# Performance work log

Measured on AMD Instinct MI355X. Metric: run time of the kernel, lower is better.

Reference implementation:

```python
import jax, jax.numpy as jnp
import numpy as np

BLOCK_SIZE = 32
BLOCK_COUNTS = 16
B, N, H, D = 4, 1024, 8, 64
LENGTHS = np.array([1024, 768, 512, 896], dtype=np.int64)


def setup_inputs() -> dict:
    key = jax.random.key(0)
    ks = jax.random.split(key, 8)
    offsets = np.concatenate([[0], np.cumsum(LENGTHS)]).astype(np.int32)
    mask = np.zeros((B, N), dtype=bool)
    for b in range(B):
        mask[b, : int(LENGTHS[b])] = True
    gather_idx = np.nonzero(mask.reshape(-1))[0].astype(np.int32)
    m = jnp.asarray(mask)[:, :, None, None].astype(jnp.float32)
    padded_q = jax.random.normal(ks[0], (B, N, H, D), jnp.float32) * m
    padded_k = jax.random.normal(ks[1], (B, N, H, D), jnp.float32) * m
    padded_v = jax.random.normal(ks[2], (B, N, H, D), jnp.float32) * m
    gidx = jnp.asarray(gather_idx)
    jagged_q = padded_q.reshape(B * N, H, D)[gidx]
    jagged_k = padded_k.reshape(B * N, H, D)[gidx]
    jagged_v = padded_v.reshape(B * N, H, D)[gidx]
    jagged_u = jax.random.normal(ks[3], (int(gidx.shape[0]), H, D), jnp.float32)
    gate_w = jax.random.normal(ks[4], (H, D, 3), jnp.float32) * 0.1
    return {"jagged_q": jagged_q, "jagged_k": jagged_k, "jagged_v": jagged_v,
            "jagged_u": jagged_u, "padded_q": padded_q, "padded_k": padded_k,
            "padded_v": padded_v, "x_offsets": jnp.asarray(offsets),
            "gate_w": gate_w, "padding_mask": jnp.asarray(mask),
            "gather_idx": gidx}


def _forward(jagged_q, jagged_k, jagged_v, padded_q, padded_k, padded_v,
             x_offsets, gate_w, gather_idx):
    scale = D ** -0.5
    nb = N // BLOCK_SIZE                                   # N is a multiple of BLOCK_SIZE (pad_len=0)
    S = min(BLOCK_COUNTS, nb)
    lengths = x_offsets[1:] - x_offsets[:-1]               # [B]
    cmp_len = (lengths + BLOCK_SIZE - 1) // BLOCK_SIZE     # [B] valid compressed blocks per seq
    pos = jnp.arange(N)
    blk = jnp.arange(nb)
    q_blk = pos // BLOCK_SIZE

    # scatter jagged tokens back to dense padded layout (zeros at padding) --
    # the Triton kernels read q/k/v from the jagged tensors.
    def to_dense(j):
        return jnp.zeros((B * N, H, D), j.dtype).at[gather_idx].set(j).reshape(B, N, H, D)
    qd, kd, vd = to_dense(jagged_q), to_dense(jagged_k), to_dense(jagged_v)

    # gates: per-token/per-head sigmoid linear gate from padded_q -> (g_cmp, g_slc, g_swa)
    gates = jax.nn.sigmoid(jnp.einsum('bnhd,hdg->bnhg', padded_q, gate_w))
    g_cmp, g_slc = gates[..., 0], gates[..., 1]            # g_swa unused by this module

    # compressed (block-mean) keys / values  [B, nb, H, D]
    k_cmp = padded_k.reshape(B, nb, BLOCK_SIZE, H, D).mean(axis=2)
    v_cmp = padded_v.reshape(B, nb, BLOCK_SIZE, H, D).mean(axis=2)

    # ---- compressed branch: SiLU attention over block-mean keys ----
    s_cmp = jnp.einsum('bqhd,bkhd->bqhk', qd, k_cmp) * scale          # [B,N,H,nb]
    mask_cmp = (q_blk[:, None] >= blk[None, :])[None, :, None, :] & \
               (blk[None, None, None, :] < cmp_len[:, None, None, None])
    p_cmp = jnp.where(mask_cmp, jax.nn.silu(s_cmp), 0.0)
    o_cmp = jnp.einsum('bqhk,bkhd->bqhd', p_cmp, v_cmp) * g_cmp[..., None]

    # ---- block selection: causal top-k over compressed scores ----
    s_sel = jnp.einsum('bqhd,bkhd->bhqk', padded_q, k_cmp) * scale    # [B,H,N,nb]
    causal_blk = (q_blk[:, None] >= blk[None, :])[None, None]
    _, top_idx = jax.lax.top_k(jnp.where(causal_blk, s_sel, -jnp.inf), S)  # [B,H,N,S]
    top_idx = jnp.where(top_idx > q_blk[None, None, :, None], -1, top_idx)
    top_idx = top_idx.transpose(0, 2, 1, 3)                           # [B,N,H,S]

    # ---- selected branch: SiLU attention restricted to selected blocks ----
    blk_sel = jnp.any(top_idx[..., None] == blk, axis=-2)             # [B,N,H,nb] (-1 matches nothing)
    key_sel = jnp.repeat(blk_sel, BLOCK_SIZE, axis=-1)                # [B,N,H,N]
    mask_slc = key_sel & (pos[:, None] >= pos[None, :])[None, :, None, :]
    s_slc = jnp.einsum('bqhd,bkhd->bqhk', qd, kd) * scale             # [B,N,H,N]
    p_slc = jnp.where(mask_slc, jax.nn.silu(s_slc), 0.0)
    o_slc = jnp.einsum('bqhk,bkhd->bqhd', p_slc, vd) * g_slc[..., None]

    # jagged output: gather valid tokens
    return (o_cmp + o_slc).reshape(B * N, H, D)[gather_idx]


def reference(jagged_q, jagged_k, jagged_v, jagged_u, padded_q, padded_k,
              padded_v, x_offsets, gate_w, padding_mask, gather_idx):
    return _forward(jagged_q, jagged_k, jagged_v, padded_q, padded_k,
                    padded_v, x_offsets, gate_w, gather_idx)
```

## Files before the change

kernel.cpp:

```cpp
#include <hip/hip_runtime.h>
#include <math.h>
#include <stdint.h>

#define BB 4
#define NN 1024
#define HH 8
#define DD 64
#define BS 32
#define NB 32
#define SS 16

typedef __attribute__((ext_vector_type(8)))  short bf16x8;
typedef __attribute__((ext_vector_type(16))) float f32x16;
typedef __attribute__((ext_vector_type(2)))  int   int2v;

union FragU { bf16x8 h; uint32_t u[4]; };

#define ZERO16 {0.f,0.f,0.f,0.f,0.f,0.f,0.f,0.f,0.f,0.f,0.f,0.f,0.f,0.f,0.f,0.f}

__device__ __forceinline__ uint32_t cvt_pk_bf16(float lo, float hi) {
    uint32_t r;
    asm("v_cvt_pk_bf16_f32 %0, %1, %2" : "=v"(r) : "v"(lo), "v"(hi));
    return r;
}

__device__ __forceinline__ float silu_f(float x) {
    return __fdividef(x, 1.f + __expf(-x));
}

__global__ __launch_bounds__(256) void cmp_mean_kernel(
    const float* __restrict__ pk, const float* __restrict__ pv,
    float* __restrict__ kc, float* __restrict__ vc)
{
    int w = threadIdx.x >> 6;
    int lane = threadIdx.x & 63;
    int idx = blockIdx.x * 4 + w;
    int r0 = lane >> 4;
    int c4 = (lane & 15) << 2;
    int h = idx & 7, blk = (idx >> 3) & 31, b = idx >> 8;
    size_t base = (((size_t)(b * NN + blk * BS + r0)) * HH + h) * DD + c4;
    float k0=0,k1=0,k2=0,k3=0,v0=0,v1=0,v2=0,v3=0;
    #pragma unroll
    for (int j = 0; j < 8; ++j) {
        const float* kp = pk + base + (size_t)j * 4 * HH * DD;
        const float* vp = pv + base + (size_t)j * 4 * HH * DD;
        float4 a = *(const float4*)kp;
        float4 c = *(const float4*)vp;
        k0+=a.x; k1+=a.y; k2+=a.z; k3+=a.w;
        v0+=c.x; v1+=c.y; v2+=c.z; v3+=c.w;
    }
    #pragma unroll
    for (int off = 16; off < 64; off <<= 1) {
        k0 += __shfl_xor(k0, off); k1 += __shfl_xor(k1, off);
        k2 += __shfl_xor(k2, off); k3 += __shfl_xor(k3, off);
        v0 += __shfl_xor(v0, off); v1 += __shfl_xor(v1, off);
        v2 += __shfl_xor(v2, off); v3 += __shfl_xor(v3, off);
    }
    if (lane < 16) {
        const float sc = 1.f / BS;
        *(float4*)(kc + (size_t)idx * DD + c4) = make_float4(k0*sc, k1*sc, k2*sc, k3*sc);
        *(float4*)(vc + (size_t)idx * DD + c4) = make_float4(v0*sc, v1*sc, v2*sc, v3*sc);
    }
}

__global__ __launch_bounds__(256, 4) void bsa_mfma_kernel(
    const float* __restrict__ pq, const float* __restrict__ pk,
    const float* __restrict__ pv, const float* __restrict__ kc,
    const float* __restrict__ vc, const float* __restrict__ gw,
    const int* __restrict__ xoff, float* __restrict__ out)
{
    __shared__ float qlds[32][64];
    __shared__ __align__(16) uint16_t pcmp[32][40];
    __shared__ uint32_t selmask[32];
    __shared__ float gateC[32], gateS[32];
    __shared__ float olds[32][64];

    const int tid = threadIdx.x;
    const int lane = tid & 63;
    const int w = tid >> 6;
    const int l31 = lane & 31;
    const int hi = lane >> 5;

    const int bid = blockIdx.x;
    const int qi = bid & 31;
    const int bh = bid >> 5;
    const int qb = (qi + bh) & 31;
    const int h = bh & 7;
    const int b = bh >> 3;

    const int off0 = xoff[b];
    const int len = xoff[b + 1] - off0;
    if (qb * BS >= len) return;

    {
        int q = tid >> 3, d = (tid & 7) * 8;
        *(float4*)&olds[q][d] = make_float4(0.f, 0.f, 0.f, 0.f);
        *(float4*)&olds[q][d + 4] = make_float4(0.f, 0.f, 0.f, 0.f);
    }

    {
        int q = tid >> 3, part = (tid & 7) * 8;
        const float* src = pq + (((size_t)(b * NN + qb * BS + q)) * HH + h) * DD + part;
        *(float4*)&qlds[q][part] = *(const float4*)src;
        *(float4*)&qlds[q][part + 4] = *(const float4*)(src + 4);
    }

    FragU qf[4];
    {
        const float* qrow = pq + (((size_t)(b * NN + qb * BS + l31)) * HH + h) * DD;
        #pragma unroll
        for (int t = 0; t < 4; ++t) {
            const float* qp = qrow + t * 16 + hi * 8;
            float4 x = *(const float4*)qp;
            float4 y = *(const float4*)(qp + 4);
            qf[t].u[0] = cvt_pk_bf16(x.x, x.y);
            qf[t].u[1] = cvt_pk_bf16(x.z, x.w);
            qf[t].u[2] = cvt_pk_bf16(y.x, y.y);
            qf[t].u[3] = cvt_pk_bf16(y.z, y.w);
        }
    }

    float4 kcv[8];
    {
        const float* kcrow = kc + (((size_t)(b * NB + l31)) * HH + h) * DD + hi * 32;
        #pragma unroll
        for (int i = 0; i < 8; ++i) kcv[i] = *(const float4*)(kcrow + i * 4);
    }

    __syncthreads();

    for (int j = 0; j < 8; ++j) {
        int q = w * 8 + j;
        const float* qv = qlds[q];
        const float* qh = qv + hi * 32;
        float part = 0.f;
        #pragma unroll
        for (int i = 0; i < 8; ++i) {
            float4 qq = *(const float4*)(qh + i * 4);
            part += qq.x * kcv[i].x + qq.y * kcv[i].y + qq.z * kcv[i].z + qq.w * kcv[i].w;
        }
        float s = (part + __shfl_xor(part, 32)) * 0.125f;
        float p = (l31 <= qb) ? silu_f(s) : 0.f;
        if (lane < 32) {
            uint32_t fb = __float_as_uint(p);
            uint16_t bp = (uint16_t)((fb + 0x7fffu + ((fb >> 16) & 1u)) >> 16);
            pcmp[q][l31] = bp;
        }
        uint32_t m;
        if (qb >= SS) {
            float vsel = (l31 <= qb) ? s : -INFINITY;
            int rank = 0;
            #pragma unroll
            for (int off = 1; off < 32; ++off) {
                float o = __shfl_xor(vsel, off);
                int oi = l31 ^ off;
                rank += (o > vsel || (o == vsel && oi < l31)) ? 1 : 0;
            }
            m = (uint32_t)(__ballot(rank < SS) & 0xffffffffu);
        } else {
            m = (1u << (qb + 1)) - 1u;
        }
        if (lane == 0) selmask[q] = m;
        float qd = qv[lane];
        float g0 = qd * gw[(h * DD + lane) * 3 + 0];
        float g1 = qd * gw[(h * DD + lane) * 3 + 1];
        #pragma unroll
        for (int off = 32; off; off >>= 1) {
            g0 += __shfl_xor(g0, off);
            g1 += __shfl_xor(g1, off);
        }
        if (lane == 0) {
            gateC[q] = __frcp_rn(1.f + __expf(-g0));
            gateS[q] = __frcp_rn(1.f + __expf(-g1));
        }
    }

    __syncthreads();

    const uint32_t mymask = selmask[l31];
    uint32_t tmask = mymask;
    #pragma unroll
    for (int off = 1; off < 32; off <<= 1) tmask |= __shfl_xor(tmask, off);

    if (w == 3) {
        f32x16 c0 = ZERO16, c1 = ZERO16;
        #pragma unroll
        for (int s = 0; s < 2; ++s) {
            FragU pa;
            pa.h = *(const bf16x8*)&pcmp[l31][s * 16 + hi * 8];
            const float* vbase = vc + (((size_t)(b * NB + s * 16 + hi * 8)) * HH + h) * DD + l31;
            #pragma unroll
            for (int dh = 0; dh < 2; ++dh) {
                FragU vb;
                #pragma unroll
                for (int jj = 0; jj < 4; ++jj) {
                    float a = vbase[(2 * jj) * 512 + dh * 32];
                    float c = vbase[(2 * jj + 1) * 512 + dh * 32];
                    vb.u[jj] = cvt_pk_bf16(a, c);
                }
                if (dh == 0) c0 = __builtin_amdgcn_mfma_f32_32x32x16_bf16(pa.h, vb.h, c0, 0, 0, 0);
                else         c1 = __builtin_amdgcn_mfma_f32_32x32x16_bf16(pa.h, vb.h, c1, 0, 0, 0);
            }
        }
        #pragma unroll
        for (int r = 0; r < 16; ++r) {
            int q = (r & 3) + 8 * (r >> 2) + 4 * hi;
            float gc = gateC[q];
            atomicAdd(&olds[q][l31], gc * c0[r]);
            atomicAdd(&olds[q][32 + l31], gc * c1[r]);
        }
    }

    f32x16 accO0 = ZERO16, accO1 = ZERO16;
    bool any = false;
    const int qpos = qb * BS + l31;
    {
        uint32_t m = tmask;
        int bcnt = 0;
        while (m) {
            int kb = __builtin_ctz(m); m &= m - 1;
            if (((bcnt++) & 3) != w) continue;
            any = true;
            f32x16 accS = ZERO16;
            const float* krow = pk + (((size_t)(b * NN + kb * BS + l31)) * HH + h) * DD;
            #pragma unroll
            for (int t = 0; t < 4; ++t) {
                const float* kp = krow + t * 16 + hi * 8;
                float4 x = *(const float4*)kp;
                float4 y = *(const float4*)(kp + 4);
                FragU kf;
                kf.u[0] = cvt_pk_bf16(x.x, x.y);
                kf.u[1] = cvt_pk_bf16(x.z, x.w);
                kf.u[2] = cvt_pk_bf16(y.x, y.y);
                kf.u[3] = cvt_pk_bf16(y.z, y.w);
                accS = __builtin_amdgcn_mfma_f32_32x32x16_bf16(kf.h, qf[t].h, accS, 0, 0, 0);
            }
            const bool selbit = (mymask >> kb) & 1;
            const bool notdiag = kb < qb;
            float pr[16];
            #pragma unroll
            for (int r = 0; r < 16; ++r) {
                int key = (r & 3) + 8 * (r >> 2) + 4 * hi;
                int kpos = kb * BS + key;
                float s = accS[r] * 0.125f;
                bool ok = selbit && (notdiag || kpos <= qpos);
                pr[r] = ok ? silu_f(s) : 0.f;
            }
            uint32_t wv[8];
            #pragma unroll
            for (int i = 0; i < 8; ++i) wv[i] = cvt_pk_bf16(pr[2 * i], pr[2 * i + 1]);
            int2v e0 = __builtin_amdgcn_permlane32_swap(wv[0], wv[2], false, false);
            int2v e1 = __builtin_amdgcn_permlane32_swap(wv[1], wv[3], false, false);
            int2v e2 = __builtin_amdgcn_permlane32_swap(wv[4], wv[6], false, false);
            int2v e3 = __builtin_amdgcn_permlane32_swap(wv[5], wv[7], false, false);
            FragU a0, a1;
            a0.u[0] = e0[0]; a0.u[1] = e1[0]; a0.u[2] = e0[1]; a0.u[3] = e1[1];
            a1.u[0] = e2[0]; a1.u[1] = e3[0]; a1.u[2] = e2[1]; a1.u[3] = e3[1];
            #pragma unroll
            for (int s = 0; s < 2; ++s) {
                const float* vbase = pv + (((size_t)(b * NN + kb * BS + s * 16 + hi * 8)) * HH + h) * DD + l31;
                const FragU& pa = s ? a1 : a0;
                #pragma unroll
                for (int dh = 0; dh < 2; ++dh) {
                    FragU vb;
                    #pragma unroll
                    for (int jj = 0; jj < 4; ++jj) {
                        float a = vbase[(2 * jj) * 512 + dh * 32];
                        float c = vbase[(2 * jj + 1) * 512 + dh * 32];
                        vb.u[jj] = cvt_pk_bf16(a, c);
                    }
                    if (dh == 0) accO0 = __builtin_amdgcn_mfma_f32_32x32x16_bf16(pa.h, vb.h, accO0, 0, 0, 0);
                    else         accO1 = __builtin_amdgcn_mfma_f32_32x32x16_bf16(pa.h, vb.h, accO1, 0, 0, 0);
                }
            }
        }
    }

    if (any) {
        #pragma unroll
        for (int r = 0; r < 16; ++r) {
            int q = (r & 3) + 8 * (r >> 2) + 4 * hi;
            float gs = gateS[q];
            atomicAdd(&olds[q][l31], gs * accO0[r]);
            atomicAdd(&olds[q][32 + l31], gs * accO1[r]);
        }
    }

    __syncthreads();

    {
        int q = tid >> 3, dpart = (tid & 7) * 8;
        int pos = qb * BS + q;
        if (pos < len) {
            float* op = out + (((size_t)(off0 + pos)) * HH + h) * DD + dpart;
            *(float4*)op = *(float4*)&olds[q][dpart];
            *(float4*)(op + 4) = *(float4*)&olds[q][dpart + 4];
        }
    }
}

extern "C" void kernel_launch(void* const* d_in, const int* in_sizes, int n_in,
                              void* d_out, int out_size, void* d_ws, size_t ws_size,
                              hipStream_t stream) {
    const float* pq = (const float*)d_in[4];
    const float* pk = (const float*)d_in[5];
    const float* pv = (const float*)d_in[6];
    const int* xoff = (const int*)d_in[7];
    const float* gw = (const float*)d_in[8];
    float* out = (float*)d_out;

    float* kc = (float*)d_ws;
    float* vc = kc + (size_t)BB * NB * HH * DD;

    cmp_mean_kernel<<<BB * NB * HH / 4, 256, 0, stream>>>(pk, pv, kc, vc);
    bsa_mfma_kernel<<<BB * HH * NB, 256, 0, stream>>>(pq, pk, pv, kc, vc, gw, xoff, out);
}
```

Before: 184.6 us.

## Precompute bf16 K and transposed V in prep kernel for direct MFMA fragment loads

The compressed-mean kernel becomes a prep kernel that also writes K as bf16 in [bh, N, D] layout and V transposed as bf16 in [bh, D, N], plus a transposed bf16 compressed V. The main attention kernel then loads MFMA fragments with single 16-byte vector loads instead of strided fp32 scalar gathers with per-element conversion. The block index mapping is also changed so heads are adjacent, which may change L2 locality. In exchange the prep pass now reads and writes the full K and V tensors, adding extra global traffic and workspace.

```diff
diff --git a/kernel.cpp b/kernel.cpp
--- a/kernel.cpp
+++ b/kernel.cpp
@@ -24,49 +24,75 @@
     return r;
 }
 
+__device__ __forceinline__ uint16_t bf16_rne(float x) {
+    uint32_t fb = __float_as_uint(x);
+    return (uint16_t)((fb + 0x7fffu + ((fb >> 16) & 1u)) >> 16);
+}
+
 __device__ __forceinline__ float silu_f(float x) {
     return __fdividef(x, 1.f + __expf(-x));
 }
 
-__global__ __launch_bounds__(256) void cmp_mean_kernel(
+__global__ __launch_bounds__(256) void prep_kernel(
     const float* __restrict__ pk, const float* __restrict__ pv,
-    float* __restrict__ kc, float* __restrict__ vc)
+    uint16_t* __restrict__ Kb, uint16_t* __restrict__ Vt,
+    float* __restrict__ kc, uint16_t* __restrict__ vct)
 {
-    int w = threadIdx.x >> 6;
-    int lane = threadIdx.x & 63;
-    int idx = blockIdx.x * 4 + w;
-    int r0 = lane >> 4;
-    int c4 = (lane & 15) << 2;
-    int h = idx & 7, blk = (idx >> 3) & 31, b = idx >> 8;
-    size_t base = (((size_t)(b * NN + blk * BS + r0)) * HH + h) * DD + c4;
-    float k0=0,k1=0,k2=0,k3=0,v0=0,v1=0,v2=0,v3=0;
-    #pragma unroll
-    for (int j = 0; j < 8; ++j) {
-        const float* kp = pk + base + (size_t)j * 4 * HH * DD;
-        const float* vp = pv + base + (size_t)j * 4 * HH * DD;
-        float4 a = *(const float4*)kp;
-        float4 c = *(const float4*)vp;
-        k0+=a.x; k1+=a.y; k2+=a.z; k3+=a.w;
-        v0+=c.x; v1+=c.y; v2+=c.z; v3+=c.w;
-    }
-    #pragma unroll
-    for (int off = 16; off < 64; off <<= 1) {
-        k0 += __shfl_xor(k0, off); k1 += __shfl_xor(k1, off);
-        k2 += __shfl_xor(k2, off); k3 += __shfl_xor(k3, off);
-        v0 += __shfl_xor(v0, off); v1 += __shfl_xor(v1, off);
-        v2 += __shfl_xor(v2, off); v3 += __shfl_xor(v3, off);
-    }
-    if (lane < 16) {
-        const float sc = 1.f / BS;
-        *(float4*)(kc + (size_t)idx * DD + c4) = make_float4(k0*sc, k1*sc, k2*sc, k3*sc);
-        *(float4*)(vc + (size_t)idx * DD + c4) = make_float4(v0*sc, v1*sc, v2*sc, v3*sc);
+    __shared__ float klds[32][65];
+    __shared__ float vlds[32][65];
+    const int t = threadIdx.x;
+    const int blk = blockIdx.x & 31;
+    const int h = (blockIdx.x >> 5) & 7;
+    const int b = blockIdx.x >> 8;
+    const int bh = b * 8 + h;
+
+    const int r = t >> 3;
+    const int dg = (t & 7) * 8;
+    size_t sbase = (((size_t)(b * NN + blk * BS + r)) * HH + h) * DD + dg;
+    float4 ka = *(const float4*)(pk + sbase);
+    float4 kb4 = *(const float4*)(pk + sbase + 4);
+    float4 va = *(const float4*)(pv + sbase);
+    float4 vb4 = *(const float4*)(pv + sbase + 4);
+
+    FragU kf;
+    kf.u[0] = cvt_pk_bf16(ka.x, ka.y);  kf.u[1] = cvt_pk_bf16(ka.z, ka.w);
+    kf.u[2] = cvt_pk_bf16(kb4.x, kb4.y); kf.u[3] = cvt_pk_bf16(kb4.z, kb4.w);
+    *(bf16x8*)(Kb + (((size_t)bh * NN) + blk * BS + r) * DD + dg) = kf.h;
+
+    *(float4*)&klds[r][dg] = ka;  *(float4*)&klds[r][dg + 4] = kb4;
+    *(float4*)&vlds[r][dg] = va;  *(float4*)&vlds[r][dg + 4] = vb4;
+    __syncthreads();
+
+    if (t < 64) {
+        float s = 0.f;
+        #pragma unroll
+        for (int j = 0; j < 32; ++j) s += klds[j][t];
+        kc[((size_t)bh * NB + blk) * DD + t] = s * (1.f / BS);
+    } else if (t < 128) {
+        int d = t - 64;
+        float s = 0.f;
+        #pragma unroll
+        for (int j = 0; j < 32; ++j) s += vlds[j][d];
+        vct[((size_t)bh * DD + d) * NB + blk] = bf16_rne(s * (1.f / BS));
+    }
+
+    {
+        int d = t >> 2, ng = (t & 3) * 8;
+        float p0 = vlds[ng + 0][d], p1 = vlds[ng + 1][d];
+        float p2 = vlds[ng + 2][d], p3 = vlds[ng + 3][d];
+        float p4 = vlds[ng + 4][d], p5 = vlds[ng + 5][d];
+        float p6 = vlds[ng + 6][d], p7 = vlds[ng + 7][d];
+        FragU vf;
+        vf.u[0] = cvt_pk_bf16(p0, p1); vf.u[1] = cvt_pk_bf16(p2, p3);
+        vf.u[2] = cvt_pk_bf16(p4, p5); vf.u[3] = cvt_pk_bf16(p6, p7);
+        *(bf16x8*)(Vt + ((size_t)bh * DD + d) * NN + blk * BS + ng) = vf.h;
     }
 }
 
 __global__ __launch_bounds__(256, 4) void bsa_mfma_kernel(
-    const float* __restrict__ pq, const float* __restrict__ pk,
-    const float* __restrict__ pv, const float* __restrict__ kc,
-    const float* __restrict__ vc, const float* __restrict__ gw,
+    const float* __restrict__ pq, const uint16_t* __restrict__ Kb,
+    const uint16_t* __restrict__ Vt, const float* __restrict__ kc,
+    const uint16_t* __restrict__ vct, const float* __restrict__ gw,
     const int* __restrict__ xoff, float* __restrict__ out)
 {
     __shared__ float qlds[32][64];
@@ -82,11 +108,11 @@
     const int hi = lane >> 5;
 
     const int bid = blockIdx.x;
-    const int qi = bid & 31;
-    const int bh = bid >> 5;
-    const int qb = (qi + bh) & 31;
-    const int h = bh & 7;
-    const int b = bh >> 3;
+    const int h = bid & 7;
+    const int rem = bid >> 3;
+    const int qb = rem & 31;
+    const int b = rem >> 5;
+    const int bh = b * 8 + h;
 
     const int off0 = xoff[b];
     const int len = xoff[b + 1] - off0;
@@ -122,7 +148,7 @@
 
     float4 kcv[8];
     {
-        const float* kcrow = kc + (((size_t)(b * NB + l31)) * HH + h) * DD + hi * 32;
+        const float* kcrow = kc + ((size_t)bh * NB + l31) * DD + hi * 32;
         #pragma unroll
         for (int i = 0; i < 8; ++i) kcv[i] = *(const float4*)(kcrow + i * 4);
     }
@@ -141,11 +167,7 @@
         }
         float s = (part + __shfl_xor(part, 32)) * 0.125f;
         float p = (l31 <= qb) ? silu_f(s) : 0.f;
-        if (lane < 32) {
-            uint32_t fb = __float_as_uint(p);
-            uint16_t bp = (uint16_t)((fb + 0x7fffu + ((fb >> 16) & 1u)) >> 16);
-            pcmp[q][l31] = bp;
-        }
+        if (lane < 32) pcmp[q][l31] = bf16_rne(p);
         uint32_t m;
         if (qb >= SS) {
             float vsel = (l31 <= qb) ? s : -INFINITY;
@@ -188,16 +210,10 @@
         for (int s = 0; s < 2; ++s) {
             FragU pa;
             pa.h = *(const bf16x8*)&pcmp[l31][s * 16 + hi * 8];
-            const float* vbase = vc + (((size_t)(b * NB + s * 16 + hi * 8)) * HH + h) * DD + l31;
             #pragma unroll
             for (int dh = 0; dh < 2; ++dh) {
                 FragU vb;
-                #pragma unroll
-                for (int jj = 0; jj < 4; ++jj) {
-                    float a = vbase[(2 * jj) * 512 + dh * 32];
-                    float c = vbase[(2 * jj + 1) * 512 + dh * 32];
-                    vb.u[jj] = cvt_pk_bf16(a, c);
-                }
+                vb.h = *(const bf16x8*)(vct + ((size_t)bh * DD + dh * 32 + l31) * NB + s * 16 + hi * 8);
                 if (dh == 0) c0 = __builtin_amdgcn_mfma_f32_32x32x16_bf16(pa.h, vb.h, c0, 0, 0, 0);
                 else         c1 = __builtin_amdgcn_mfma_f32_32x32x16_bf16(pa.h, vb.h, c1, 0, 0, 0);
             }
@@ -222,17 +238,11 @@
             if (((bcnt++) & 3) != w) continue;
             any = true;
             f32x16 accS = ZERO16;
-            const float* krow = pk + (((size_t)(b * NN + kb * BS + l31)) * HH + h) * DD;
+            const uint16_t* krow = Kb + (((size_t)bh * NN) + kb * BS + l31) * DD;
             #pragma unroll
             for (int t = 0; t < 4; ++t) {
-                const float* kp = krow + t * 16 + hi * 8;
-                float4 x = *(const float4*)kp;
-                float4 y = *(const float4*)(kp + 4);
                 FragU kf;
-                kf.u[0] = cvt_pk_bf16(x.x, x.y);
-                kf.u[1] = cvt_pk_bf16(x.z, x.w);
-                kf.u[2] = cvt_pk_bf16(y.x, y.y);
-                kf.u[3] = cvt_pk_bf16(y.z, y.w);
+                kf.h = *(const bf16x8*)(krow + t * 16 + hi * 8);
                 accS = __builtin_amdgcn_mfma_f32_32x32x16_bf16(kf.h, qf[t].h, accS, 0, 0, 0);
             }
             const bool selbit = (mymask >> kb) & 1;
@@ -258,17 +268,11 @@
             a1.u[0] = e2[0]; a1.u[1] = e3[0]; a1.u[2] = e2[1]; a1.u[3] = e3[1];
             #pragma unroll
             for (int s = 0; s < 2; ++s) {
-                const float* vbase = pv + (((size_t)(b * NN + kb * BS + s * 16 + hi * 8)) * HH + h) * DD + l31;
                 const FragU& pa = s ? a1 : a0;
                 #pragma unroll
                 for (int dh = 0; dh < 2; ++dh) {
                     FragU vb;
-                    #pragma unroll
-                    for (int jj = 0; jj < 4; ++jj) {
-                        float a = vbase[(2 * jj) * 512 + dh * 32];
-                        float c = vbase[(2 * jj + 1) * 512 + dh * 32];
-                        vb.u[jj] = cvt_pk_bf16(a, c);
-                    }
+                    vb.h = *(const bf16x8*)(Vt + ((size_t)bh * DD + dh * 32 + l31) * NN + kb * BS + s * 16 + hi * 8);
                     if (dh == 0) accO0 = __builtin_amdgcn_mfma_f32_32x32x16_bf16(pa.h, vb.h, accO0, 0, 0, 0);
                     else         accO1 = __builtin_amdgcn_mfma_f32_32x32x16_bf16(pa.h, vb.h, accO1, 0, 0, 0);
                 }
@@ -309,9 +313,11 @@
     const float* gw = (const float*)d_in[8];
     float* out = (float*)d_out;
 
-    float* kc = (float*)d_ws;
-    float* vc = kc + (size_t)BB * NB * HH * DD;
-
-    cmp_mean_kernel<<<BB * NB * HH / 4, 256, 0, stream>>>(pk, pv, kc, vc);
-    bsa_mfma_kernel<<<BB * HH * NB, 256, 0, stream>>>(pq, pk, pv, kc, vc, gw, xoff, out);
-}
+    uint16_t* Kb = (uint16_t*)d_ws;
+    uint16_t* Vt = Kb + (size_t)BB * HH * NN * DD;
+    float* kc = (float*)(Vt + (size_t)BB * HH * NN * DD);
+    uint16_t* vct = (uint16_t*)(kc + (size_t)BB * HH * NB * DD);
+
+    prep_kernel<<<BB * HH * NB, 256, 0, stream>>>(pk, pv, Kb, Vt, kc, vct);
+    bsa_mfma_kernel<<<BB * HH * NB, 256, 0, stream>>>(pq, Kb, Vt, kc, vct, gw, xoff, out);
+}
```

New measurement: 173.8 us. 1.06x faster.
